# Kernel optimization log

Measured on AMD Instinct MI355X. Metric: run time of the kernel, lower is better.

Reference implementation:

```python
import jax, jax.numpy as jnp
import numpy as np

B, T, D, H, E, O = 4, 2048, 512, 2048, 4, 512
C = 1024  # expert capacity
HE = H // E  # per-expert hidden width


def setup_inputs() -> dict:
    key = jax.random.key(0)
    ks = jax.random.split(key, 7)
    x = jax.random.normal(ks[0], (B, T, D), dtype=jnp.float32)
    dispatch_mask = jax.random.uniform(ks[1], (B, T, E, C), dtype=jnp.float32)
    combine_array = jax.random.uniform(ks[2], (B, T, E, C), dtype=jnp.float32)
    # per-expert parameters (fc1 contract, fc2 expand)
    w1 = jax.random.normal(ks[3], (E, D, HE), dtype=jnp.float32) * (1.0 / np.sqrt(D))
    b1 = jnp.zeros((E, HE), dtype=jnp.float32)
    w2 = jax.random.normal(ks[4], (E, HE, O), dtype=jnp.float32) * (1.0 / np.sqrt(HE))
    b2 = jnp.zeros((O,), dtype=jnp.float32)
    return {"x": x, "dispatch_mask": dispatch_mask, "combine_array": combine_array,
            "w1": w1, "b1": b1, "w2": w2, "b2": b2}


def reference(x, dispatch_mask, combine_array, w1, b1, w2, b2):
    # dispatch: gather tokens into per-expert capacity buffers [B,E,C,D]
    xd = jnp.einsum('btd,btec->becd', x, dispatch_mask)
    # per-expert fc1: [B,E,C,HE]
    h = jnp.einsum('becd,edh->bech', xd, w1) + b1[None, :, None, :]
    # GELU (exact erf form, matching torch nn.GELU default); norm/dropout are identity
    h = jax.nn.gelu(h, approximate=False)
    # per-expert fc2: [B,E,C,O]
    y = jnp.einsum('bech,eho->beco', h, w2)
    # combine: scatter expert outputs back to tokens [B,T,O]
    out = jnp.einsum('beco,btec->bto', y, combine_array) + b2
    return out
```

## Files before the change

### kernel.cpp

```cpp
#include <hip/hip_runtime.h>
#include <math.h>

namespace {

typedef short short8 __attribute__((ext_vector_type(8)));
typedef float f32x4 __attribute__((ext_vector_type(4)));

constexpr int kB = 4, kT = 2048, kD = 512, kE = 4, kC = 1024, kHE = 512,
              kO = 512, kEC = 4096;

__device__ __forceinline__ unsigned short f2bf(float f) {
    unsigned int u = __float_as_uint(f);
    u += 0x7fffu + ((u >> 16) & 1u);
    return (unsigned short)(u >> 16);
}

__device__ __forceinline__ float gelu_exact(float v) {
    return 0.5f * v * (1.0f + erff(v * 0.70710678118654752f));
}

#define GLDS16(g, l)                                                      \
    __builtin_amdgcn_global_load_lds(                                     \
        (const __attribute__((address_space(1))) unsigned int*)(g),       \
        (__attribute__((address_space(3))) unsigned int*)(l), 16, 0, 0)

__global__ __launch_bounds__(256)
void transpose_cast(const float* __restrict__ in, unsigned short* __restrict__ out,
                    int R, int Cc, long long sIn, long long sOut)
{
    __shared__ float tile[32][33];
    const int z = blockIdx.z;
    const float* ip = in + (long long)z * sIn;
    unsigned short* op = out + (long long)z * sOut;
    const int c0 = blockIdx.x * 32, r0 = blockIdx.y * 32;
    const int tx = threadIdx.x & 31, ty = threadIdx.x >> 5;
#pragma unroll
    for (int i = 0; i < 4; ++i) {
        const int r = ty + i * 8;
        tile[r][tx] = ip[(size_t)(r0 + r) * Cc + c0 + tx];
    }
    __syncthreads();
#pragma unroll
    for (int i = 0; i < 4; ++i) {
        const int c = ty + i * 8;
        op[(size_t)(c0 + c) * R + r0 + tx] = f2bf(tile[tx][c]);
    }
}

__global__ __launch_bounds__(256)
void cast_bf16(const float* __restrict__ in, unsigned short* __restrict__ out,
               long long n)
{
    const long long i = ((long long)blockIdx.x * blockDim.x + threadIdx.x) * 4;
    if (i < n) {
        const float4 v = *(const float4*)&in[i];
        unsigned short o[4] = {f2bf(v.x), f2bf(v.y), f2bf(v.z), f2bf(v.w)};
        *(uint2*)&out[i] = *(const uint2*)o;
    }
}

template <int MODE>
__global__ __launch_bounds__(256)
void mfma_gemm(const unsigned short* __restrict__ Aall,
               const unsigned short* __restrict__ Ball,
               const float* __restrict__ biasAll,
               void* __restrict__ Call,
               int M, int N, int K,
               long long sA, long long sB, long long sC,
               int zModA, int zModB, int zModBias, int biasStride, int bShift)
{
    __shared__ unsigned short As[128 * 64];
    __shared__ unsigned short Bs[128 * 64];

    const int z = blockIdx.z;
    const unsigned short* Ab = Aall + (long long)(z % zModA) * sA;
    const unsigned short* Bb = Ball + (long long)(z % zModB) * sB;
    const float* bias =
        (MODE != 0) ? biasAll + (long long)(z % zModBias) * biasStride : nullptr;

    const int t = threadIdx.x;
    const int lane = t & 63;
    const int w = t >> 6;
    const int wrow = w * 32;
    const int l8r = lane >> 3;
    const int l8c = (lane & 7) * 8;
    const int row0 = blockIdx.y * 128;
    const int col0 = blockIdx.x * 128;

    const int wm = (w >> 1) * 64;
    const int wn = (w & 1) * 64;
    const int fr = lane & 15;
    const int fq = (lane >> 4) * 8;

    const unsigned int bMask = (1u << bShift) - 1u;

    f32x4 acc[4][4] = {};

    for (int k0 = 0; k0 < K; k0 += 64) {
#pragma unroll
        for (int r = 0; r < 4; ++r) {
            const int ar = row0 + wrow + r * 8 + l8r;
            GLDS16(Ab + (size_t)ar * K + (k0 + l8c), &As[(wrow + r * 8) * 64]);
            const int bn = col0 + wrow + r * 8 + l8r;
            const int gk = k0 + l8c;
            const size_t boff =
                (((size_t)(gk >> bShift) * N + bn) << bShift) + (gk & bMask);
            GLDS16(Bb + boff, &Bs[(wrow + r * 8) * 64]);
        }
        __syncthreads();
#pragma unroll
        for (int kk = 0; kk < 2; ++kk) {
            short8 af[4], bf[4];
#pragma unroll
            for (int i = 0; i < 4; ++i)
                af[i] = *(const short8*)&As[(wm + i * 16 + fr) * 64 + kk * 32 + fq];
#pragma unroll
            for (int j = 0; j < 4; ++j)
                bf[j] = *(const short8*)&Bs[(wn + j * 16 + fr) * 64 + kk * 32 + fq];
#pragma unroll
            for (int i = 0; i < 4; ++i)
#pragma unroll
                for (int j = 0; j < 4; ++j)
                    acc[i][j] = __builtin_amdgcn_mfma_f32_16x16x32_bf16(
                        af[i], bf[j], acc[i][j], 0, 0, 0);
        }
        __syncthreads();
    }

    const long long cz = (long long)z * sC;
#pragma unroll
    for (int i = 0; i < 4; ++i) {
        const int rowb = row0 + wm + i * 16 + (lane >> 4) * 4;
#pragma unroll
        for (int j = 0; j < 4; ++j) {
            const int col = col0 + wn + j * 16 + fr;
            const float bv = (MODE != 0) ? bias[col] : 0.0f;
#pragma unroll
            for (int r = 0; r < 4; ++r) {
                const float v = acc[i][j][r];
                const size_t idx = (size_t)cz + (size_t)(rowb + r) * N + col;
                if (MODE == 0)
                    ((unsigned short*)Call)[idx] = f2bf(v);
                else if (MODE == 1)
                    ((unsigned short*)Call)[idx] = f2bf(gelu_exact(v + bv));
                else
                    ((float*)Call)[idx] = v + bv;
            }
        }
    }
}

}

extern "C" void kernel_launch(void* const* d_in, const int* in_sizes, int n_in,
                              void* d_out, int out_size, void* d_ws, size_t ws_size,
                              hipStream_t stream)
{
    const float* x    = (const float*)d_in[0];
    const float* mask = (const float*)d_in[1];
    const float* comb = (const float*)d_in[2];
    const float* w1   = (const float*)d_in[3];
    const float* b1   = (const float*)d_in[4];
    const float* w2   = (const float*)d_in[5];
    const float* b2   = (const float*)d_in[6];
    float* out = (float*)d_out;

    unsigned short* ws    = (unsigned short*)d_ws;
    unsigned short* regA  = ws;
    unsigned short* xT    = regA + 33554432;
    unsigned short* w1T   = xT + 4194304;
    unsigned short* w2T   = w1T + 1048576;
    unsigned short* xd    = w2T + 1048576;
    unsigned short* h     = xd + 8388608;
    unsigned short* maskT = regA;
    unsigned short* combB = regA;
    unsigned short* yT    = xd;

    dim3 blk(256);

    transpose_cast<<<dim3(kEC / 32, kT / 32, kB), blk, 0, stream>>>(
        mask, maskT, kT, kEC, (long long)kT * kEC, (long long)kT * kEC);
    transpose_cast<<<dim3(kD / 32, kT / 32, kB), blk, 0, stream>>>(
        x, xT, kT, kD, (long long)kT * kD, (long long)kT * kD);
    transpose_cast<<<dim3(kHE / 32, kD / 32, kE), blk, 0, stream>>>(
        w1, w1T, kD, kHE, (long long)kD * kHE, (long long)kD * kHE);
    transpose_cast<<<dim3(kO / 32, kHE / 32, kE), blk, 0, stream>>>(
        w2, w2T, kHE, kO, (long long)kHE * kO, (long long)kHE * kO);

    mfma_gemm<0><<<dim3(kD / 128, kEC / 128, kB), blk, 0, stream>>>(
        maskT, xT, nullptr, xd, kEC, kD, kT,
        (long long)kEC * kT, (long long)kD * kT, (long long)kEC * kD,
        kB, kB, 1, 0, 11);

    cast_bf16<<<dim3(33554432 / 4 / 256), blk, 0, stream>>>(
        comb, combB, 33554432LL);

    mfma_gemm<1><<<dim3(kHE / 128, kC / 128, kB * kE), blk, 0, stream>>>(
        xd, w1T, b1, h, kC, kHE, kD,
        (long long)kC * kD, (long long)kHE * kD, (long long)kC * kHE,
        kB * kE, kE, kE, kHE, 9);

    mfma_gemm<0><<<dim3(kC / 128, kO / 128, kB * kE), blk, 0, stream>>>(
        w2T, h, nullptr, yT, kO, kC, kHE,
        (long long)kO * kHE, (long long)kC * kHE, (long long)kO * kC,
        kE, kB * kE, 1, 0, 9);

    mfma_gemm<3><<<dim3(kO / 128, kT / 128, kB), blk, 0, stream>>>(
        combB, yT, b2, out, kT, kO, kEC,
        (long long)kT * kEC, (long long)kE * kO * kC, (long long)kT * kO,
        kB, kB, 1, 0, 10);
}
```

Before: 500.9 us.

## Split-K the dispatch and combine GEMMs with atomic accumulation and block swizzle

The dispatch GEMM is split 2-way along K and the combine GEMM 4-way. Partial results are accumulated with float atomics into a zero- or bias-initialised fp32 buffer. The change also adds a flat-index block remapping that interleaves work across groups of 8, and the fc1 GEMM now reads the fp32 dispatch output and casts it to bf16 while loading A. The aim is more blocks in flight for the low-grid, long-K GEMMs. The cost is extra fill kernels, atomic traffic, an fp32 intermediate and nondeterministic summation order.

```diff
diff --git a/kernel.cpp b/kernel.cpp
--- a/kernel.cpp
+++ b/kernel.cpp
@@ -59,24 +59,55 @@
     }
 }
 
-template <int MODE>
-__global__ __launch_bounds__(256)
-void mfma_gemm(const unsigned short* __restrict__ Aall,
+__global__ __launch_bounds__(256)
+void fill_zero(float* __restrict__ p, long long n4)
+{
+    const long long i = (long long)blockIdx.x * blockDim.x + threadIdx.x;
+    if (i < n4) *(float4*)&p[i * 4] = make_float4(0.f, 0.f, 0.f, 0.f);
+}
+
+__global__ __launch_bounds__(256)
+void fill_bias(float* __restrict__ p, const float* __restrict__ b2, long long n4)
+{
+    const long long i = (long long)blockIdx.x * blockDim.x + threadIdx.x;
+    if (i < n4) {
+        const int col = (int)((i * 4) & (kO - 1));
+        *(float4*)&p[i * 4] = *(const float4*)&b2[col];
+    }
+}
+
+template <int MODE, bool AF32>
+__global__ __launch_bounds__(256)
+void mfma_gemm(const void* __restrict__ Aall,
                const unsigned short* __restrict__ Ball,
                const float* __restrict__ biasAll,
                void* __restrict__ Call,
-               int M, int N, int K,
+               int M, int N, int Kext, int KA,
                long long sA, long long sB, long long sC,
-               int zModA, int zModB, int zModBias, int biasStride, int bShift)
+               int zModA, int zModB, int zModBias, int biasStride,
+               int bShift, int kSplit)
 {
     __shared__ unsigned short As[128 * 64];
     __shared__ unsigned short Bs[128 * 64];
 
-    const int z = blockIdx.z;
-    const unsigned short* Ab = Aall + (long long)(z % zModA) * sA;
-    const unsigned short* Bb = Ball + (long long)(z % zModB) * sB;
+    const int nt = gridDim.x, mt = gridDim.y;
+    const int flat = blockIdx.x + nt * (blockIdx.y + mt * blockIdx.z);
+    const int total = nt * mt * gridDim.z;
+    const int work = (flat & 7) * (total >> 3) + (flat >> 3);
+    const int z = work / (mt * nt);
+    const int rem = work - z * (mt * nt);
+    const int my = rem / nt;
+    const int nx = rem - my * nt;
+
+    const int zz = z / kSplit;
+    const int ks = z - zz * kSplit;
+    const int kBeg = ks * Kext;
+
+    const unsigned short* Ab =
+        (const unsigned short*)Aall + (long long)(zz % zModA) * sA;
+    const unsigned short* Bb = Ball + (long long)(zz % zModB) * sB;
     const float* bias =
-        (MODE != 0) ? biasAll + (long long)(z % zModBias) * biasStride : nullptr;
+        (MODE == 1) ? biasAll + (long long)(zz % zModBias) * biasStride : nullptr;
 
     const int t = threadIdx.x;
     const int lane = t & 63;
@@ -84,27 +115,42 @@
     const int wrow = w * 32;
     const int l8r = lane >> 3;
     const int l8c = (lane & 7) * 8;
-    const int row0 = blockIdx.y * 128;
-    const int col0 = blockIdx.x * 128;
+    const int row0 = my * 128;
+    const int col0 = nx * 128;
 
     const int wm = (w >> 1) * 64;
     const int wn = (w & 1) * 64;
     const int fr = lane & 15;
     const int fq = (lane >> 4) * 8;
 
-    const unsigned int bMask = (1u << bShift) - 1u;
-
     f32x4 acc[4][4] = {};
 
-    for (int k0 = 0; k0 < K; k0 += 64) {
+    for (int k0 = 0; k0 < Kext; k0 += 64) {
+        if (AF32) {
+            const float* Af = (const float*)Aall + (long long)(zz % zModA) * sA;
+#pragma unroll
+            for (int r = 0; r < 8; ++r) {
+                const int f = r * 256 + t;
+                const int row = f >> 4;
+                const int k4 = (f & 15) * 4;
+                const float4 v = *(const float4*)
+                    &Af[(size_t)(row0 + row) * KA + kBeg + k0 + k4];
+                unsigned short o[4] = {f2bf(v.x), f2bf(v.y), f2bf(v.z), f2bf(v.w)};
+                *(uint2*)&As[row * 64 + k4] = *(const uint2*)o;
+            }
+        }
 #pragma unroll
         for (int r = 0; r < 4; ++r) {
-            const int ar = row0 + wrow + r * 8 + l8r;
-            GLDS16(Ab + (size_t)ar * K + (k0 + l8c), &As[(wrow + r * 8) * 64]);
+            if (!AF32) {
+                const int ar = row0 + wrow + r * 8 + l8r;
+                GLDS16(Ab + (size_t)ar * KA + (kBeg + k0 + l8c),
+                       &As[(wrow + r * 8) * 64]);
+            }
             const int bn = col0 + wrow + r * 8 + l8r;
-            const int gk = k0 + l8c;
+            const int gk = kBeg + k0 + l8c;
             const size_t boff =
-                (((size_t)(gk >> bShift) * N + bn) << bShift) + (gk & bMask);
+                (((size_t)(gk >> bShift) * N + bn) << bShift) +
+                (gk & ((1u << bShift) - 1u));
             GLDS16(Bb + boff, &Bs[(wrow + r * 8) * 64]);
         }
         __syncthreads();
@@ -127,14 +173,14 @@
         __syncthreads();
     }
 
-    const long long cz = (long long)z * sC;
+    const long long cz = (long long)zz * sC;
 #pragma unroll
     for (int i = 0; i < 4; ++i) {
         const int rowb = row0 + wm + i * 16 + (lane >> 4) * 4;
 #pragma unroll
         for (int j = 0; j < 4; ++j) {
             const int col = col0 + wn + j * 16 + fr;
-            const float bv = (MODE != 0) ? bias[col] : 0.0f;
+            const float bv = (MODE == 1) ? bias[col] : 0.0f;
 #pragma unroll
             for (int r = 0; r < 4; ++r) {
                 const float v = acc[i][j][r];
@@ -144,7 +190,7 @@
                 else if (MODE == 1)
                     ((unsigned short*)Call)[idx] = f2bf(gelu_exact(v + bv));
                 else
-                    ((float*)Call)[idx] = v + bv;
+                    unsafeAtomicAdd(&((float*)Call)[idx], v);
             }
         }
     }
@@ -165,16 +211,15 @@
     const float* b2   = (const float*)d_in[6];
     float* out = (float*)d_out;
 
-    unsigned short* ws    = (unsigned short*)d_ws;
-    unsigned short* regA  = ws;
+    unsigned short* regA  = (unsigned short*)d_ws;
     unsigned short* xT    = regA + 33554432;
     unsigned short* w1T   = xT + 4194304;
     unsigned short* w2T   = w1T + 1048576;
-    unsigned short* xd    = w2T + 1048576;
-    unsigned short* h     = xd + 8388608;
+    float*          xdF   = (float*)(w2T + 1048576);
+    unsigned short* h     = (unsigned short*)(xdF + 8388608);
     unsigned short* maskT = regA;
     unsigned short* combB = regA;
-    unsigned short* yT    = xd;
+    unsigned short* yT    = (unsigned short*)xdF;
 
     dim3 blk(256);
 
@@ -186,27 +231,29 @@
         w1, w1T, kD, kHE, (long long)kD * kHE, (long long)kD * kHE);
     transpose_cast<<<dim3(kO / 32, kHE / 32, kE), blk, 0, stream>>>(
         w2, w2T, kHE, kO, (long long)kHE * kO, (long long)kHE * kO);
-
-    mfma_gemm<0><<<dim3(kD / 128, kEC / 128, kB), blk, 0, stream>>>(
-        maskT, xT, nullptr, xd, kEC, kD, kT,
+    fill_zero<<<dim3(8388608 / 4 / 256), blk, 0, stream>>>(xdF, 8388608LL / 4);
+
+    mfma_gemm<2, false><<<dim3(kD / 128, kEC / 128, kB * 2), blk, 0, stream>>>(
+        maskT, xT, nullptr, xdF, kEC, kD, kT / 2, kT,
         (long long)kEC * kT, (long long)kD * kT, (long long)kEC * kD,
-        kB, kB, 1, 0, 11);
+        kB, kB, 1, 0, 11, 2);
 
     cast_bf16<<<dim3(33554432 / 4 / 256), blk, 0, stream>>>(
         comb, combB, 33554432LL);
 
-    mfma_gemm<1><<<dim3(kHE / 128, kC / 128, kB * kE), blk, 0, stream>>>(
-        xd, w1T, b1, h, kC, kHE, kD,
+    mfma_gemm<1, true><<<dim3(kHE / 128, kC / 128, kB * kE), blk, 0, stream>>>(
+        xdF, w1T, b1, h, kC, kHE, kD, kD,
         (long long)kC * kD, (long long)kHE * kD, (long long)kC * kHE,
-        kB * kE, kE, kE, kHE, 9);
-
-    mfma_gemm<0><<<dim3(kC / 128, kO / 128, kB * kE), blk, 0, stream>>>(
-        w2T, h, nullptr, yT, kO, kC, kHE,
+        kB * kE, kE, kE, kHE, 9, 1);
+
+    mfma_gemm<0, false><<<dim3(kC / 128, kO / 128, kB * kE), blk, 0, stream>>>(
+        w2T, h, nullptr, yT, kO, kC, kHE, kHE,
         (long long)kO * kHE, (long long)kC * kHE, (long long)kO * kC,
-        kE, kB * kE, 1, 0, 9);
-
-    mfma_gemm<3><<<dim3(kO / 128, kT / 128, kB), blk, 0, stream>>>(
-        combB, yT, b2, out, kT, kO, kEC,
+        kE, kB * kE, 1, 0, 9, 1);
+
+    fill_bias<<<dim3(4194304 / 4 / 256), blk, 0, stream>>>(out, b2, 4194304LL / 4);
+    mfma_gemm<2, false><<<dim3(kO / 128, kT / 128, kB * 4), blk, 0, stream>>>(
+        combB, yT, b2, out, kT, kO, kEC / 4, kEC,
         (long long)kT * kEC, (long long)kE * kO * kC, (long long)kT * kO,
-        kB, kB, 1, 0, 10);
-}
+        kB, kB, 1, 0, 10, 4);
+}
```

Result: slower. 552.6 us (+10.3%).
